# Kernel optimization log

Measured on AMD Instinct MI355X. Metric: run time of the kernel, lower is better.

## Reference

```python
import jax, jax.numpy as jnp
import numpy as np

N, E, D, ED, H = 50000, 640000, 128, 64, 128
EPS = 1e-5


def _bn(x, gamma, beta):
    # BatchNorm1d in training mode: batch stats over rows, biased variance
    mean = jnp.mean(x, axis=0)
    var = jnp.mean(jnp.square(x - mean), axis=0)
    return (x - mean) * jax.lax.rsqrt(var + EPS) * gamma + beta


def setup_inputs() -> dict:
    key = jax.random.key(0)
    ks = jax.random.split(key, 12)

    def lin(k, fan_in, fan_out):
        return jax.random.normal(k, (fan_in, fan_out), jnp.float32) / np.sqrt(fan_in)

    return {
        "h": jax.random.normal(ks[0], (N, D), jnp.float32),
        "edge_attr": jax.random.normal(ks[1], (E, ED), jnp.float32),
        # msg MLP: Linear(2D+ED->H), BN(H), ReLU, Linear(H->H)
        "W1": lin(ks[2], 2 * D + ED, H), "b1": jnp.zeros((H,), jnp.float32),
        "g1": jnp.ones((H,), jnp.float32), "be1": jnp.zeros((H,), jnp.float32),
        "W2": lin(ks[3], H, H), "b2": jnp.zeros((H,), jnp.float32),
        # upd MLP: Linear(D+H->H), BN(H), ReLU, Linear(H->D)
        "W3": lin(ks[4], D + H, H), "b3": jnp.zeros((H,), jnp.float32),
        "g2": jnp.ones((H,), jnp.float32), "be2": jnp.zeros((H,), jnp.float32),
        "W4": lin(ks[5], H, D), "b4": jnp.zeros((D,), jnp.float32),
        # residual LayerNorm
        "ln_g": jnp.ones((D,), jnp.float32), "ln_b": jnp.zeros((D,), jnp.float32),
        "edge_index": jax.random.randint(ks[6], (2, E), 0, N, jnp.int32),
        "num_nodes": N,
    }


def reference(h, edge_attr, W1, b1, g1, be1, W2, b2, W3, b3, g2, be2, W4, b4,
              ln_g, ln_b, edge_index, num_nodes):
    src, dst = edge_index[0], edge_index[1]
    # messages: MLP_msg(h_src || h_dst || e)  -> [E, H]
    msg_in = jnp.concatenate([h[src], h[dst], edge_attr], axis=-1)  # [E, 2D+ED]
    x = _bn(msg_in @ W1 + b1, g1, be1)
    messages = jax.nn.relu(x) @ W2 + b2
    # scatter-sum aggregate into dst nodes -> [N, H]
    agg = jax.ops.segment_sum(messages, dst, num_segments=num_nodes)
    # update: MLP_upd(h || agg) -> [N, D]
    u = jnp.concatenate([h, agg], axis=-1)
    y = _bn(u @ W3 + b3, g2, be2)
    h_new = jax.nn.relu(y) @ W4 + b4
    # residual + LayerNorm
    z = h + h_new
    mu = jnp.mean(z, axis=-1, keepdims=True)
    var = jnp.mean(jnp.square(z - mu), axis=-1, keepdims=True)
    return (z - mu) * jax.lax.rsqrt(var + EPS) * ln_g + ln_b
```

## Files before the change

kernel.cpp:

```cpp
#include <hip/hip_runtime.h>
#include <hip/hip_bf16.h>

#define EPS 1e-5f
#define DIMH 128
#define K1 320
#define K3 256

typedef __attribute__((ext_vector_type(8))) short bf16x8;
typedef __attribute__((ext_vector_type(4))) short bf16x4;
typedef __attribute__((ext_vector_type(4))) float f32x4;

#define MFMA(a, b, c) __builtin_amdgcn_mfma_f32_16x16x32_bf16(a, b, c, 0, 0, 0)

static __device__ __forceinline__ unsigned short f2bf(float f) {
    union { float f; unsigned u; } v; v.f = f;
    unsigned r = v.u + 0x7FFF + ((v.u >> 16) & 1);
    return (unsigned short)(r >> 16);
}

static __device__ __forceinline__ void gload16(const void* g, void* l) {
    __builtin_amdgcn_global_load_lds(
        (const __attribute__((address_space(1))) unsigned int*)g,
        (__attribute__((address_space(3))) unsigned int*)l, 16, 0, 0);
}

__global__ void k_prep_w(const float* __restrict__ W1, const float* __restrict__ W3,
                         const float* __restrict__ W4,
                         unsigned short* __restrict__ W1t, unsigned short* __restrict__ W3c,
                         unsigned short* __restrict__ W4t) {
    int t = blockIdx.x * 256 + threadIdx.x;
    if (t < K1 * 128) { int k = t / 128, n = t % 128; W1t[n * K1 + k] = f2bf(W1[t]); }
    if (t < 128 * 128) {
        int k = t / 128, n = t % 128;
        W4t[n * 128 + k] = f2bf(W4[t]);
        W3c[n * K3 + k] = f2bf(W3[t]);
    }
}

__global__ void k_hb(const float* __restrict__ h, unsigned short* __restrict__ hb, int total8) {
    int t = blockIdx.x * 256 + threadIdx.x;
    if (t < total8) {
        float4 a = *(const float4*)(h + (size_t)t * 8);
        float4 b = *(const float4*)(h + (size_t)t * 8 + 4);
        union { bf16x8 v; unsigned short s[8]; } u;
        u.s[0] = f2bf(a.x); u.s[1] = f2bf(a.y); u.s[2] = f2bf(a.z); u.s[3] = f2bf(a.w);
        u.s[4] = f2bf(b.x); u.s[5] = f2bf(b.y); u.s[6] = f2bf(b.z); u.s[7] = f2bf(b.w);
        *(bf16x8*)(hb + (size_t)t * 8) = u.v;
    }
}

__global__ void k_w23(const float* __restrict__ W2, const float* __restrict__ W3,
                      unsigned short* __restrict__ W3c) {
    int t = blockIdx.x * 256 + threadIdx.x;
    int j = t & 127, i = t >> 7;
    float s = 0.f;
    for (int k = 0; k < 128; ++k) s += W2[i * 128 + k] * W3[(128 + k) * 128 + j];
    W3c[j * K3 + 128 + i] = f2bf(s);
}

__global__ void k_cvec(const float* __restrict__ b2, const float* __restrict__ W3,
                       float* __restrict__ cvec) {
    int j = threadIdx.x;
    float s = 0.f;
    for (int k = 0; k < 128; ++k) s += b2[k] * W3[(128 + k) * 128 + j];
    cvec[j] = s;
}

__global__ void k_bn(const float* __restrict__ stats, const float* __restrict__ g,
                     const float* __restrict__ be, float* __restrict__ st, float cnt) {
    int c = threadIdx.x;
    float mean = stats[c] / cnt;
    float var = stats[128 + c] / cnt - mean * mean;
    float s = g[c] * rsqrtf(var + EPS);
    st[c] = s;
    st[128 + c] = be[c] - mean * s;
}

__global__ void k_deg(const int* __restrict__ dst, int* __restrict__ deg, int E) {
    int e = blockIdx.x * 256 + threadIdx.x;
    if (e < E) atomicAdd(&deg[dst[e]], 1);
}

__global__ void k_scan(const int* __restrict__ deg, int* __restrict__ offs,
                       int* __restrict__ cursor, int NN) {
    __shared__ int ps[1024];
    int t = threadIdx.x;
    int chunk = (NN + 1023) >> 10;
    int c0 = t * chunk;
    int s = 0;
    for (int i = 0; i < chunk; ++i) { int id = c0 + i; if (id < NN) s += deg[id]; }
    ps[t] = s; __syncthreads();
    for (int off = 1; off < 1024; off <<= 1) {
        int v = (t >= off) ? ps[t - off] : 0;
        __syncthreads();
        ps[t] += v;
        __syncthreads();
    }
    int run = t ? ps[t - 1] : 0;
    for (int i = 0; i < chunk; ++i) {
        int id = c0 + i;
        if (id < NN) { cursor[id] = run; run += deg[id]; offs[id] = run; }
    }
}

__global__ void k_scatter(const int* __restrict__ dst, int* __restrict__ cursor,
                          int* __restrict__ elist, int E) {
    int e = blockIdx.x * 256 + threadIdx.x;
    if (e < E) {
        int pos = atomicAdd(&cursor[dst[e]], 1);
        elist[pos] = e;
    }
}

__global__ __launch_bounds__(256, 3) void k_msg1(
    const unsigned short* __restrict__ hb, const float* __restrict__ ea,
    const int* __restrict__ src, const int* __restrict__ dst,
    const unsigned short* __restrict__ W1t, const float* __restrict__ b1,
    unsigned short* __restrict__ xout, float* __restrict__ stats) {
    __shared__ unsigned short As[64 * 128];
    __shared__ unsigned short Ad[64 * 128];
    __shared__ unsigned short Ae[64 * 64];
    int tid = threadIdx.x, lane = tid & 63, w = tid >> 6;
    int l15 = lane & 15, kq = lane >> 4;
    long e0 = (long)blockIdx.x * 64;

    bf16x8 bfr[10][2];
    {
        int n = (w << 5) + l15, kb = kq << 3;
#pragma unroll
        for (int nt = 0; nt < 2; ++nt) {
            const unsigned short* p = W1t + (size_t)(n + nt * 16) * K1 + kb;
#pragma unroll
            for (int ks = 0; ks < 10; ++ks) bfr[ks][nt] = *(const bf16x8*)(p + ks * 32);
        }
    }
    {
#pragma unroll
        for (int j = 0; j < 4; ++j) {
            int r4 = (w << 4) + j * 4;
            int row = r4 + kq;
            int u = l15 ^ (row & 7);
            long e = e0 + row;
            int sI = src[e], dI = dst[e];
            gload16(hb + (size_t)sI * 128 + u * 8, &As[r4 * 128]);
            gload16(hb + (size_t)dI * 128 + u * 8, &Ad[r4 * 128]);
        }
    }
    {
        int s8 = lane & 7, rq8 = lane >> 3;
#pragma unroll
        for (int p = 0; p < 2; ++p) {
            int row = (w << 4) + p * 8 + rq8;
            int u = (s8 ^ (row & 7)) << 3;
            const float* ep = ea + (size_t)(e0 + row) * 64 + u;
            float4 va = *(const float4*)ep;
            float4 vb = *(const float4*)(ep + 4);
            union { bf16x8 v; unsigned short s[8]; } uu;
            uu.s[0] = f2bf(va.x); uu.s[1] = f2bf(va.y); uu.s[2] = f2bf(va.z); uu.s[3] = f2bf(va.w);
            uu.s[4] = f2bf(vb.x); uu.s[5] = f2bf(vb.y); uu.s[6] = f2bf(vb.z); uu.s[7] = f2bf(vb.w);
            *(bf16x8*)&Ae[row * 64 + s8 * 8] = uu.v;
        }
    }
    __syncthreads();

    f32x4 acc[4][2] = {};
#pragma unroll
    for (int rg = 0; rg < 4; ++rg) {
        int a = rg * 16 + l15;
        int swz = a & 7;
        const unsigned short* pAs = As + a * 128;
        const unsigned short* pAd = Ad + a * 128;
        const unsigned short* pAe = Ae + a * 64;
#pragma unroll
        for (int ks = 0; ks < 4; ++ks) {
            bf16x8 af = *(const bf16x8*)(pAs + (((ks << 2) + kq) ^ swz) * 8);
            acc[rg][0] = MFMA(af, bfr[ks][0], acc[rg][0]);
            acc[rg][1] = MFMA(af, bfr[ks][1], acc[rg][1]);
        }
#pragma unroll
        for (int ks = 0; ks < 4; ++ks) {
            bf16x8 af = *(const bf16x8*)(pAd + (((ks << 2) + kq) ^ swz) * 8);
            acc[rg][0] = MFMA(af, bfr[4 + ks][0], acc[rg][0]);
            acc[rg][1] = MFMA(af, bfr[4 + ks][1], acc[rg][1]);
        }
#pragma unroll
        for (int ks = 0; ks < 2; ++ks) {
            bf16x8 af = *(const bf16x8*)(pAe + (((ks << 2) + kq) ^ swz) * 8);
            acc[rg][0] = MFMA(af, bfr[8 + ks][0], acc[rg][0]);
            acc[rg][1] = MFMA(af, bfr[8 + ks][1], acc[rg][1]);
        }
    }
    __syncthreads();
    unsigned short* xt = As;
    int c0 = (w << 5) + l15;
    float bias0 = b1[c0], bias1 = b1[c0 + 16];
    float ss0 = 0.f, ss1 = 0.f, sq0 = 0.f, sq1 = 0.f;
#pragma unroll
    for (int rg = 0; rg < 4; ++rg)
#pragma unroll
        for (int r = 0; r < 4; ++r) {
            int row = rg * 16 + (kq << 2) + r;
            float v0 = acc[rg][0][r] + bias0;
            float v1 = acc[rg][1][r] + bias1;
            ss0 += v0; sq0 += v0 * v0;
            ss1 += v1; sq1 += v1 * v1;
            xt[row * 128 + c0] = f2bf(v0);
            xt[row * 128 + c0 + 16] = f2bf(v1);
        }
    __syncthreads();
#pragma unroll
    for (int p = 0; p < 4; ++p) {
        int off8 = p * 2048 + tid * 8;
        *(bf16x8*)(xout + (size_t)e0 * 128 + off8) = *(const bf16x8*)(xt + off8);
    }
    ss0 += __shfl_xor(ss0, 16); ss0 += __shfl_xor(ss0, 32);
    sq0 += __shfl_xor(sq0, 16); sq0 += __shfl_xor(sq0, 32);
    ss1 += __shfl_xor(ss1, 16); ss1 += __shfl_xor(ss1, 32);
    sq1 += __shfl_xor(sq1, 16); sq1 += __shfl_xor(sq1, 32);
    if (lane < 16) {
        atomicAdd(&stats[c0], ss0);        atomicAdd(&stats[c0 + 16], ss1);
        atomicAdd(&stats[128 + c0], sq0);  atomicAdd(&stats[128 + c0 + 16], sq1);
    }
}

__global__ __launch_bounds__(256, 8) void k_agg(
    const unsigned short* __restrict__ x, const float* __restrict__ st,
    const int* __restrict__ offs, const int* __restrict__ deg,
    const int* __restrict__ elist, float* __restrict__ R, int NN) {
    int lane = threadIdx.x & 63, w = threadIdx.x >> 6;
    int n = blockIdx.x * 4 + w;
    if (n >= NN) return;
    int c = lane * 2;
    float s0 = st[c], s1 = st[c + 1], t0 = st[128 + c], t1 = st[128 + c + 1];
    int end = offs[n], i = end - deg[n];
    float a0 = 0.f, a1 = 0.f;
    for (; i + 3 < end; i += 4) {
        int e0 = elist[i], e1 = elist[i + 1], e2 = elist[i + 2], e3 = elist[i + 3];
        unsigned v0 = *(const unsigned*)(x + (size_t)e0 * DIMH + c);
        unsigned v1 = *(const unsigned*)(x + (size_t)e1 * DIMH + c);
        unsigned v2 = *(const unsigned*)(x + (size_t)e2 * DIMH + c);
        unsigned v3 = *(const unsigned*)(x + (size_t)e3 * DIMH + c);
        a0 += fmaxf(__uint_as_float(v0 << 16) * s0 + t0, 0.f);
        a1 += fmaxf(__uint_as_float(v0 & 0xffff0000u) * s1 + t1, 0.f);
        a0 += fmaxf(__uint_as_float(v1 << 16) * s0 + t0, 0.f);
        a1 += fmaxf(__uint_as_float(v1 & 0xffff0000u) * s1 + t1, 0.f);
        a0 += fmaxf(__uint_as_float(v2 << 16) * s0 + t0, 0.f);
        a1 += fmaxf(__uint_as_float(v2 & 0xffff0000u) * s1 + t1, 0.f);
        a0 += fmaxf(__uint_as_float(v3 << 16) * s0 + t0, 0.f);
        a1 += fmaxf(__uint_as_float(v3 & 0xffff0000u) * s1 + t1, 0.f);
    }
    for (; i < end; ++i) {
        int e0 = elist[i];
        unsigned v0 = *(const unsigned*)(x + (size_t)e0 * DIMH + c);
        a0 += fmaxf(__uint_as_float(v0 << 16) * s0 + t0, 0.f);
        a1 += fmaxf(__uint_as_float(v0 & 0xffff0000u) * s1 + t1, 0.f);
    }
    *(float2*)(R + (size_t)n * DIMH + c) = make_float2(a0, a1);
}

__global__ __launch_bounds__(256, 3) void k_upd1(
    const unsigned short* __restrict__ hb, const float* __restrict__ R,
    const unsigned short* __restrict__ W3c, const float* __restrict__ b3,
    const int* __restrict__ deg, const float* __restrict__ cvec,
    unsigned short* __restrict__ ypre, float* __restrict__ stats, int NN) {
    __shared__ unsigned short A[64 * K3];
    int tid = threadIdx.x, lane = tid & 63, w = tid >> 6;
    int n0 = blockIdx.x * 64;

    bf16x8 bfr[8][2];
    {
        int n = (w << 5) + (lane & 15), kb = (lane >> 4) << 3;
#pragma unroll
        for (int nt = 0; nt < 2; ++nt) {
            const unsigned short* p = W3c + (size_t)(n + nt * 16) * K3 + kb;
#pragma unroll
            for (int ks = 0; ks < 8; ++ks) bfr[ks][nt] = *(const bf16x8*)(p + ks * 32);
        }
    }
    {
        int c16 = tid & 15, r2 = tid >> 4;
#pragma unroll
        for (int rr = 0; rr < 4; ++rr) {
            int row = rr * 16 + r2;
            int node = n0 + row;
            bf16x8 vh = {};
            union { bf16x8 v8; unsigned short s8[8]; } ur;
            if (node < NN) {
                vh = *(const bf16x8*)(hb + (size_t)node * DIMH + c16 * 8);
                float4 r0 = *(const float4*)(R + (size_t)node * DIMH + c16 * 8);
                float4 r1 = *(const float4*)(R + (size_t)node * DIMH + c16 * 8 + 4);
                ur.s8[0] = f2bf(r0.x); ur.s8[1] = f2bf(r0.y); ur.s8[2] = f2bf(r0.z); ur.s8[3] = f2bf(r0.w);
                ur.s8[4] = f2bf(r1.x); ur.s8[5] = f2bf(r1.y); ur.s8[6] = f2bf(r1.z); ur.s8[7] = f2bf(r1.w);
            } else {
#pragma unroll
                for (int j = 0; j < 8; ++j) ur.s8[j] = 0;
            }
            int base = row * K3, sw = (row & 7) << 3;
            *(bf16x8*)&A[(base + c16 * 8) ^ sw] = vh;
            *(bf16x8*)&A[(base + 128 + c16 * 8) ^ sw] = ur.v8;
        }
    }
    __syncthreads();

    f32x4 acc[4][2] = {};
#pragma unroll
    for (int rg = 0; rg < 4; ++rg) {
        int arow = rg * 16 + (lane & 15);
        int base = arow * K3, sw = (arow & 7) << 3, kb = (lane >> 4) << 3;
#pragma unroll
        for (int ks = 0; ks < 8; ++ks) {
            bf16x8 af = *(const bf16x8*)&A[(base + ks * 32 + kb) ^ sw];
            acc[rg][0] = MFMA(af, bfr[ks][0], acc[rg][0]);
            acc[rg][1] = MFMA(af, bfr[ks][1], acc[rg][1]);
        }
    }
    int c0 = (w << 5) + (lane & 15);
    float bias0 = b3[c0], bias1 = b3[c0 + 16];
    float cv0 = cvec[c0], cv1 = cvec[c0 + 16];
    float ss[2] = {0.f, 0.f}, sq[2] = {0.f, 0.f};
#pragma unroll
    for (int rg = 0; rg < 4; ++rg)
#pragma unroll
        for (int r = 0; r < 4; ++r) {
            int node = n0 + rg * 16 + ((lane >> 4) << 2) + r;
            if (node < NN) {
                float dg = (float)deg[node];
                float v0 = acc[rg][0][r] + bias0 + dg * cv0;
                float v1 = acc[rg][1][r] + bias1 + dg * cv1;
                ss[0] += v0; sq[0] += v0 * v0;
                ss[1] += v1; sq[1] += v1 * v1;
                ypre[(size_t)node * DIMH + c0] = f2bf(v0);
                ypre[(size_t)node * DIMH + c0 + 16] = f2bf(v1);
            }
        }
#pragma unroll
    for (int nt = 0; nt < 2; ++nt) {
        ss[nt] += __shfl_xor(ss[nt], 16); ss[nt] += __shfl_xor(ss[nt], 32);
        sq[nt] += __shfl_xor(sq[nt], 16); sq[nt] += __shfl_xor(sq[nt], 32);
    }
    if (lane < 16) {
        atomicAdd(&stats[c0], ss[0]);        atomicAdd(&stats[c0 + 16], ss[1]);
        atomicAdd(&stats[128 + c0], sq[0]);  atomicAdd(&stats[128 + c0 + 16], sq[1]);
    }
}

__global__ __launch_bounds__(256, 2) void k_upd2(
    const unsigned short* __restrict__ ypre, const unsigned short* __restrict__ W4t,
    const float* __restrict__ b4, const float* __restrict__ st,
    const float* __restrict__ h, const float* __restrict__ lng,
    const float* __restrict__ lnb, float* __restrict__ out, int NN) {
    const int LDA = 136;
    __shared__ unsigned short A[64 * 136];
    __shared__ float sS[128], sT[128];
    __shared__ float rsum[64], rsq[64];
    int tid = threadIdx.x, lane = tid & 63, w = tid >> 6;
    int n0 = blockIdx.x * 64;
    if (tid < 128) { sS[tid] = st[tid]; sT[tid] = st[128 + tid]; }
    if (tid < 64) { rsum[tid] = 0.f; rsq[tid] = 0.f; }

    bf16x8 bfr[4][2];
    {
        int n = (w << 5) + (lane & 15), kb = (lane >> 4) << 3;
#pragma unroll
        for (int nt = 0; nt < 2; ++nt) {
            const unsigned short* p = W4t + (size_t)(n + nt * 16) * 128 + kb;
#pragma unroll
            for (int ks = 0; ks < 4; ++ks) bfr[ks][nt] = *(const bf16x8*)(p + ks * 32);
        }
    }
    __syncthreads();
    {
        int c16 = tid & 15, r2 = tid >> 4;
#pragma unroll
        for (int rr = 0; rr < 4; ++rr) {
            int row = rr * 16 + r2;
            int node = n0 + row;
            union { bf16x8 v8; unsigned short s[8]; } u;
            if (node < NN) {
                bf16x8 v = *(const bf16x8*)(ypre + (size_t)node * DIMH + c16 * 8);
#pragma unroll
                for (int j = 0; j < 8; ++j) {
                    int c = c16 * 8 + j;
                    union { unsigned uu; float f; } cvt; cvt.uu = ((unsigned)(unsigned short)v[j]) << 16;
                    float f = cvt.f * sS[c] + sT[c];
                    u.s[j] = f2bf(fmaxf(f, 0.f));
                }
            } else {
#pragma unroll
                for (int j = 0; j < 8; ++j) u.s[j] = 0;
            }
            *(bf16x8*)&A[row * LDA + c16 * 8] = u.v8;
        }
    }
    __syncthreads();

    f32x4 acc[4][2] = {};
#pragma unroll
    for (int rg = 0; rg < 4; ++rg) {
        int ab = (rg * 16 + (lane & 15)) * LDA + ((lane >> 4) << 3);
#pragma unroll
        for (int ks = 0; ks < 4; ++ks) {
            bf16x8 af = *(const bf16x8*)&A[ab + ks * 32];
            acc[rg][0] = MFMA(af, bfr[ks][0], acc[rg][0]);
            acc[rg][1] = MFMA(af, bfr[ks][1], acc[rg][1]);
        }
    }
    int c0 = (w << 5) + (lane & 15);
    float bias0 = b4[c0], bias1 = b4[c0 + 16];
    float z[4][2][4];
#pragma unroll
    for (int rg = 0; rg < 4; ++rg)
#pragma unroll
        for (int r = 0; r < 4; ++r) {
            int node = n0 + rg * 16 + ((lane >> 4) << 2) + r;
            float h0 = 0.f, h1 = 0.f;
            if (node < NN) {
                h0 = h[(size_t)node * DIMH + c0];
                h1 = h[(size_t)node * DIMH + c0 + 16];
            }
            z[rg][0][r] = acc[rg][0][r] + bias0 + h0;
            z[rg][1][r] = acc[rg][1][r] + bias1 + h1;
        }
#pragma unroll
    for (int rg = 0; rg < 4; ++rg)
#pragma unroll
        for (int r = 0; r < 4; ++r) {
            float ps = z[rg][0][r] + z[rg][1][r];
            float pq = z[rg][0][r] * z[rg][0][r] + z[rg][1][r] * z[rg][1][r];
#pragma unroll
            for (int m = 1; m < 16; m <<= 1) { ps += __shfl_xor(ps, m); pq += __shfl_xor(pq, m); }
            if ((lane & 15) == 0) {
                int row = rg * 16 + ((lane >> 4) << 2) + r;
                atomicAdd(&rsum[row], ps);
                atomicAdd(&rsq[row], pq);
            }
        }
    __syncthreads();
#pragma unroll
    for (int rg = 0; rg < 4; ++rg)
#pragma unroll
        for (int r = 0; r < 4; ++r) {
            int row = rg * 16 + ((lane >> 4) << 2) + r;
            int node = n0 + row;
            if (node < NN) {
                float mean = rsum[row] * (1.f / 128.f);
                float var = rsq[row] * (1.f / 128.f) - mean * mean;
                float rs = rsqrtf(var + EPS);
                float g0 = lng[c0], g1 = lng[c0 + 16];
                float be0 = lnb[c0], be1 = lnb[c0 + 16];
                out[(size_t)node * DIMH + c0] = (z[rg][0][r] - mean) * rs * g0 + be0;
                out[(size_t)node * DIMH + c0 + 16] = (z[rg][1][r] - mean) * rs * g1 + be1;
            }
        }
}

extern "C" void kernel_launch(void* const* d_in, const int* in_sizes, int n_in,
                              void* d_out, int out_size, void* d_ws, size_t ws_size,
                              hipStream_t stream) {
    const float* h   = (const float*)d_in[0];
    const float* ea  = (const float*)d_in[1];
    const float* W1  = (const float*)d_in[2];
    const float* b1  = (const float*)d_in[3];
    const float* g1  = (const float*)d_in[4];
    const float* be1 = (const float*)d_in[5];
    const float* W2  = (const float*)d_in[6];
    const float* b2  = (const float*)d_in[7];
    const float* W3  = (const float*)d_in[8];
    const float* b3  = (const float*)d_in[9];
    const float* g2  = (const float*)d_in[10];
    const float* be2 = (const float*)d_in[11];
    const float* W4  = (const float*)d_in[12];
    const float* b4  = (const float*)d_in[13];
    const float* lng = (const float*)d_in[14];
    const float* lnb = (const float*)d_in[15];
    const int* eidx  = (const int*)d_in[16];
    int NN = in_sizes[0] / DIMH;
    int E  = in_sizes[16] / 2;
    const int* src = eidx;
    const int* dst = eidx + E;

    char* ws = (char*)d_ws;
    size_t o = 0;
    unsigned short* W1t = (unsigned short*)(ws + o); o += 81920;
    unsigned short* W3c = (unsigned short*)(ws + o); o += 65536;
    unsigned short* W4t = (unsigned short*)(ws + o); o += 32768;
    float* cvec   = (float*)(ws + o); o += 512;
    float* stats1 = (float*)(ws + o); o += 1024;
    float* st1    = (float*)(ws + o); o += 1024;
    float* stats2 = (float*)(ws + o); o += 1024;
    float* st2    = (float*)(ws + o); o += 1024;
    int* deg    = (int*)(ws + o); o += 200192;
    int* offs   = (int*)(ws + o); o += 200192;
    int* cursor = (int*)(ws + o); o += 200192;
    int* elist  = (int*)(ws + o); o += (size_t)E * 4;
    unsigned short* hb = (unsigned short*)(ws + o); o += (size_t)NN * DIMH * 2;
    float* R = (float*)(ws + o); o += (size_t)NN * DIMH * 4;
    unsigned short* x = (unsigned short*)(ws + o);
    unsigned short* ypre = x;

    hipMemsetAsync(stats1, 0, 1024, stream);
    hipMemsetAsync(stats2, 0, 1024, stream);
    hipMemsetAsync(deg, 0, (size_t)NN * 4, stream);

    k_prep_w<<<(K1 * 128 + 255) / 256, 256, 0, stream>>>(W1, W3, W4, W1t, W3c, W4t);
    k_hb<<<(NN * DIMH / 8 + 255) / 256, 256, 0, stream>>>(h, hb, NN * DIMH / 8);
    k_w23<<<64, 256, 0, stream>>>(W2, W3, W3c);
    k_cvec<<<1, 128, 0, stream>>>(b2, W3, cvec);
    k_deg<<<(E + 255) / 256, 256, 0, stream>>>(dst, deg, E);
    k_scan<<<1, 1024, 0, stream>>>(deg, offs, cursor, NN);
    k_scatter<<<(E + 255) / 256, 256, 0, stream>>>(dst, cursor, elist, E);

    k_msg1<<<E / 64, 256, 0, stream>>>(hb, ea, src, dst, W1t, b1, x, stats1);
    k_bn<<<1, 128, 0, stream>>>(stats1, g1, be1, st1, (float)E);
    k_agg<<<(NN + 3) / 4, 256, 0, stream>>>(x, st1, offs, deg, elist, R, NN);

    int nb = (NN + 63) / 64;
    k_upd1<<<nb, 256, 0, stream>>>(hb, R, W3c, b3, deg, cvec, ypre, stats2, NN);
    k_bn<<<1, 128, 0, stream>>>(stats2, g2, be2, st2, (float)NN);
    k_upd2<<<nb, 256, 0, stream>>>(ypre, W4t, b4, st2, h, lng, lnb, (float*)d_out, NN);
}
```

Baseline: 812.6 us.

## Process edges in dst-sorted order so aggregation reads contiguous message rows

```diff
diff --git a/kernel.cpp b/kernel.cpp
--- a/kernel.cpp
+++ b/kernel.cpp
@@ -81,42 +81,69 @@
     if (e < E) atomicAdd(&deg[dst[e]], 1);
 }
 
-__global__ void k_scan(const int* __restrict__ deg, int* __restrict__ offs,
-                       int* __restrict__ cursor, int NN) {
-    __shared__ int ps[1024];
+__global__ void k_part(const int* __restrict__ deg, int* __restrict__ bsum, int NN) {
+    __shared__ int s[256];
+    int t = threadIdx.x, g = blockIdx.x * 256 + t;
+    s[t] = (g < NN) ? deg[g] : 0;
+    __syncthreads();
+    for (int o = 128; o > 0; o >>= 1) { if (t < o) s[t] += s[t + o]; __syncthreads(); }
+    if (t == 0) bsum[blockIdx.x] = s[0];
+}
+
+__global__ void k_scan2(const int* __restrict__ bsum, int* __restrict__ bpre, int nb) {
+    __shared__ int s[256];
     int t = threadIdx.x;
-    int chunk = (NN + 1023) >> 10;
-    int c0 = t * chunk;
-    int s = 0;
-    for (int i = 0; i < chunk; ++i) { int id = c0 + i; if (id < NN) s += deg[id]; }
-    ps[t] = s; __syncthreads();
-    for (int off = 1; off < 1024; off <<= 1) {
-        int v = (t >= off) ? ps[t - off] : 0;
+    int v = (t < nb) ? bsum[t] : 0;
+    s[t] = v; __syncthreads();
+    for (int o = 1; o < 256; o <<= 1) {
+        int u = (t >= o) ? s[t - o] : 0;
         __syncthreads();
-        ps[t] += v;
+        s[t] += u;
         __syncthreads();
     }
-    int run = t ? ps[t - 1] : 0;
-    for (int i = 0; i < chunk; ++i) {
-        int id = c0 + i;
-        if (id < NN) { cursor[id] = run; run += deg[id]; offs[id] = run; }
-    }
-}
-
-__global__ void k_scatter(const int* __restrict__ dst, int* __restrict__ cursor,
-                          int* __restrict__ elist, int E) {
+    if (t < nb) bpre[t] = s[t] - v;
+}
+
+__global__ void k_off(const int* __restrict__ deg, const int* __restrict__ bpre,
+                      int* __restrict__ offs, int* __restrict__ cursor, int NN) {
+    __shared__ int s[256];
+    int t = threadIdx.x, g = blockIdx.x * 256 + t;
+    int v = (g < NN) ? deg[g] : 0;
+    s[t] = v; __syncthreads();
+    for (int o = 1; o < 256; o <<= 1) {
+        int u = (t >= o) ? s[t - o] : 0;
+        __syncthreads();
+        s[t] += u;
+        __syncthreads();
+    }
+    if (g < NN) {
+        int incl = s[t] + bpre[blockIdx.x];
+        offs[g] = incl;
+        cursor[g] = incl - v;
+    }
+}
+
+__global__ void k_scatter(const int* __restrict__ src, const int* __restrict__ dst,
+                          int* __restrict__ cursor, int4* __restrict__ edge4, int E) {
     int e = blockIdx.x * 256 + threadIdx.x;
     if (e < E) {
-        int pos = atomicAdd(&cursor[dst[e]], 1);
-        elist[pos] = e;
-    }
-}
-
-__global__ __launch_bounds__(256, 3) void k_msg1(
-    const unsigned short* __restrict__ hb, const float* __restrict__ ea,
-    const int* __restrict__ src, const int* __restrict__ dst,
-    const unsigned short* __restrict__ W1t, const float* __restrict__ b1,
-    unsigned short* __restrict__ xout, float* __restrict__ stats) {
+        int d = dst[e];
+        int pos = atomicAdd(&cursor[d], 1);
+        edge4[pos] = make_int4(src[e], d, e, 0);
+    }
+}
+
+#define QSTEP(PTR, FIDX, BA, BB) do { \
+    bf16x8 af = *(const bf16x8*)((PTR) + ((((FIDX)) ^ swz) << 3)); \
+    acc[rg][0] = MFMA(af, BA, acc[rg][0]); \
+    acc[rg][1] = MFMA(af, BB, acc[rg][1]); } while (0)
+
+__global__ __launch_bounds__(256)
+__attribute__((amdgpu_waves_per_eu(2, 3)))
+void k_msg1(const unsigned short* __restrict__ hb, const float* __restrict__ ea,
+            const int4* __restrict__ edge4, const unsigned short* __restrict__ W1t,
+            const float* __restrict__ b1, unsigned short* __restrict__ xout,
+            float* __restrict__ stats) {
     __shared__ unsigned short As[64 * 128];
     __shared__ unsigned short Ad[64 * 128];
     __shared__ unsigned short Ae[64 * 64];
@@ -124,35 +151,45 @@
     int l15 = lane & 15, kq = lane >> 4;
     long e0 = (long)blockIdx.x * 64;
 
-    bf16x8 bfr[10][2];
+    bf16x8 B0a, B1a, B2a, B3a, B4a, B5a, B6a, B7a, B8a, B9a;
+    bf16x8 B0b, B1b, B2b, B3b, B4b, B5b, B6b, B7b, B8b, B9b;
     {
         int n = (w << 5) + l15, kb = kq << 3;
-#pragma unroll
-        for (int nt = 0; nt < 2; ++nt) {
-            const unsigned short* p = W1t + (size_t)(n + nt * 16) * K1 + kb;
-#pragma unroll
-            for (int ks = 0; ks < 10; ++ks) bfr[ks][nt] = *(const bf16x8*)(p + ks * 32);
-        }
-    }
-    {
-#pragma unroll
-        for (int j = 0; j < 4; ++j) {
-            int r4 = (w << 4) + j * 4;
-            int row = r4 + kq;
-            int u = l15 ^ (row & 7);
-            long e = e0 + row;
-            int sI = src[e], dI = dst[e];
-            gload16(hb + (size_t)sI * 128 + u * 8, &As[r4 * 128]);
-            gload16(hb + (size_t)dI * 128 + u * 8, &Ad[r4 * 128]);
-        }
+        const unsigned short* p0 = W1t + (size_t)n * K1 + kb;
+        const unsigned short* p1 = p0 + 16 * K1;
+        B0a = *(const bf16x8*)(p0 + 0);   B0b = *(const bf16x8*)(p1 + 0);
+        B1a = *(const bf16x8*)(p0 + 32);  B1b = *(const bf16x8*)(p1 + 32);
+        B2a = *(const bf16x8*)(p0 + 64);  B2b = *(const bf16x8*)(p1 + 64);
+        B3a = *(const bf16x8*)(p0 + 96);  B3b = *(const bf16x8*)(p1 + 96);
+        B4a = *(const bf16x8*)(p0 + 128); B4b = *(const bf16x8*)(p1 + 128);
+        B5a = *(const bf16x8*)(p0 + 160); B5b = *(const bf16x8*)(p1 + 160);
+        B6a = *(const bf16x8*)(p0 + 192); B6b = *(const bf16x8*)(p1 + 192);
+        B7a = *(const bf16x8*)(p0 + 224); B7b = *(const bf16x8*)(p1 + 224);
+        B8a = *(const bf16x8*)(p0 + 256); B8b = *(const bf16x8*)(p1 + 256);
+        B9a = *(const bf16x8*)(p0 + 288); B9b = *(const bf16x8*)(p1 + 288);
+    }
+    asm volatile("" : "+v"(B0a), "+v"(B1a), "+v"(B2a), "+v"(B3a), "+v"(B4a),
+                      "+v"(B5a), "+v"(B6a), "+v"(B7a), "+v"(B8a), "+v"(B9a));
+    asm volatile("" : "+v"(B0b), "+v"(B1b), "+v"(B2b), "+v"(B3b), "+v"(B4b),
+                      "+v"(B5b), "+v"(B6b), "+v"(B7b), "+v"(B8b), "+v"(B9b));
+
+#pragma unroll
+    for (int j = 0; j < 4; ++j) {
+        int r4 = (w << 4) + j * 4;
+        int row = r4 + kq;
+        int4 ei = edge4[e0 + row];
+        int u = l15 ^ (row & 7);
+        gload16(hb + (size_t)ei.x * 128 + u * 8, &As[r4 * 128]);
+        gload16(hb + (size_t)ei.y * 128 + u * 8, &Ad[r4 * 128]);
     }
     {
         int s8 = lane & 7, rq8 = lane >> 3;
 #pragma unroll
         for (int p = 0; p < 2; ++p) {
             int row = (w << 4) + p * 8 + rq8;
+            int eid = edge4[e0 + row].z;
             int u = (s8 ^ (row & 7)) << 3;
-            const float* ep = ea + (size_t)(e0 + row) * 64 + u;
+            const float* ep = ea + (size_t)eid * 64 + u;
             float4 va = *(const float4*)ep;
             float4 vb = *(const float4*)(ep + 4);
             union { bf16x8 v; unsigned short s[8]; } uu;
@@ -171,24 +208,16 @@
         const unsigned short* pAs = As + a * 128;
         const unsigned short* pAd = Ad + a * 128;
         const unsigned short* pAe = Ae + a * 64;
-#pragma unroll
-        for (int ks = 0; ks < 4; ++ks) {
-            bf16x8 af = *(const bf16x8*)(pAs + (((ks << 2) + kq) ^ swz) * 8);
-            acc[rg][0] = MFMA(af, bfr[ks][0], acc[rg][0]);
-            acc[rg][1] = MFMA(af, bfr[ks][1], acc[rg][1]);
-        }
-#pragma unroll
-        for (int ks = 0; ks < 4; ++ks) {
-            bf16x8 af = *(const bf16x8*)(pAd + (((ks << 2) + kq) ^ swz) * 8);
-            acc[rg][0] = MFMA(af, bfr[4 + ks][0], acc[rg][0]);
-            acc[rg][1] = MFMA(af, bfr[4 + ks][1], acc[rg][1]);
-        }
-#pragma unroll
-        for (int ks = 0; ks < 2; ++ks) {
-            bf16x8 af = *(const bf16x8*)(pAe + (((ks << 2) + kq) ^ swz) * 8);
-            acc[rg][0] = MFMA(af, bfr[8 + ks][0], acc[rg][0]);
-            acc[rg][1] = MFMA(af, bfr[8 + ks][1], acc[rg][1]);
-        }
+        QSTEP(pAs, (0 << 2) + kq, B0a, B0b);
+        QSTEP(pAs, (1 << 2) + kq, B1a, B1b);
+        QSTEP(pAs, (2 << 2) + kq, B2a, B2b);
+        QSTEP(pAs, (3 << 2) + kq, B3a, B3b);
+        QSTEP(pAd, (0 << 2) + kq, B4a, B4b);
+        QSTEP(pAd, (1 << 2) + kq, B5a, B5b);
+        QSTEP(pAd, (2 << 2) + kq, B6a, B6b);
+        QSTEP(pAd, (3 << 2) + kq, B7a, B7b);
+        QSTEP(pAe, (0 << 2) + kq, B8a, B8b);
+        QSTEP(pAe, (1 << 2) + kq, B9a, B9b);
     }
     __syncthreads();
     unsigned short* xt = As;
@@ -226,7 +255,7 @@
 __global__ __launch_bounds__(256, 8) void k_agg(
     const unsigned short* __restrict__ x, const float* __restrict__ st,
     const int* __restrict__ offs, const int* __restrict__ deg,
-    const int* __restrict__ elist, float* __restrict__ R, int NN) {
+    float* __restrict__ R, int NN) {
     int lane = threadIdx.x & 63, w = threadIdx.x >> 6;
     int n = blockIdx.x * 4 + w;
     if (n >= NN) return;
@@ -234,24 +263,16 @@
     float s0 = st[c], s1 = st[c + 1], t0 = st[128 + c], t1 = st[128 + c + 1];
     int end = offs[n], i = end - deg[n];
     float a0 = 0.f, a1 = 0.f;
-    for (; i + 3 < end; i += 4) {
-        int e0 = elist[i], e1 = elist[i + 1], e2 = elist[i + 2], e3 = elist[i + 3];
-        unsigned v0 = *(const unsigned*)(x + (size_t)e0 * DIMH + c);
-        unsigned v1 = *(const unsigned*)(x + (size_t)e1 * DIMH + c);
-        unsigned v2 = *(const unsigned*)(x + (size_t)e2 * DIMH + c);
-        unsigned v3 = *(const unsigned*)(x + (size_t)e3 * DIMH + c);
+    for (; i + 1 < end; i += 2) {
+        unsigned v0 = *(const unsigned*)(x + (size_t)i * DIMH + c);
+        unsigned v1 = *(const unsigned*)(x + (size_t)(i + 1) * DIMH + c);
         a0 += fmaxf(__uint_as_float(v0 << 16) * s0 + t0, 0.f);
         a1 += fmaxf(__uint_as_float(v0 & 0xffff0000u) * s1 + t1, 0.f);
         a0 += fmaxf(__uint_as_float(v1 << 16) * s0 + t0, 0.f);
         a1 += fmaxf(__uint_as_float(v1 & 0xffff0000u) * s1 + t1, 0.f);
-        a0 += fmaxf(__uint_as_float(v2 << 16) * s0 + t0, 0.f);
-        a1 += fmaxf(__uint_as_float(v2 & 0xffff0000u) * s1 + t1, 0.f);
-        a0 += fmaxf(__uint_as_float(v3 << 16) * s0 + t0, 0.f);
-        a1 += fmaxf(__uint_as_float(v3 & 0xffff0000u) * s1 + t1, 0.f);
-    }
-    for (; i < end; ++i) {
-        int e0 = elist[i];
-        unsigned v0 = *(const unsigned*)(x + (size_t)e0 * DIMH + c);
+    }
+    if (i < end) {
+        unsigned v0 = *(const unsigned*)(x + (size_t)i * DIMH + c);
         a0 += fmaxf(__uint_as_float(v0 << 16) * s0 + t0, 0.f);
         a1 += fmaxf(__uint_as_float(v0 & 0xffff0000u) * s1 + t1, 0.f);
     }
@@ -489,10 +510,12 @@
     float* st1    = (float*)(ws + o); o += 1024;
     float* stats2 = (float*)(ws + o); o += 1024;
     float* st2    = (float*)(ws + o); o += 1024;
+    int* bsum   = (int*)(ws + o); o += 1024;
+    int* bpre   = (int*)(ws + o); o += 1024;
     int* deg    = (int*)(ws + o); o += 200192;
     int* offs   = (int*)(ws + o); o += 200192;
     int* cursor = (int*)(ws + o); o += 200192;
-    int* elist  = (int*)(ws + o); o += (size_t)E * 4;
+    int4* edge4 = (int4*)(ws + o); o += (size_t)E * 16;
     unsigned short* hb = (unsigned short*)(ws + o); o += (size_t)NN * DIMH * 2;
     float* R = (float*)(ws + o); o += (size_t)NN * DIMH * 4;
     unsigned short* x = (unsigned short*)(ws + o);
@@ -502,17 +525,20 @@
     hipMemsetAsync(stats2, 0, 1024, stream);
     hipMemsetAsync(deg, 0, (size_t)NN * 4, stream);
 
+    int nb256 = (NN + 255) / 256;
     k_prep_w<<<(K1 * 128 + 255) / 256, 256, 0, stream>>>(W1, W3, W4, W1t, W3c, W4t);
     k_hb<<<(NN * DIMH / 8 + 255) / 256, 256, 0, stream>>>(h, hb, NN * DIMH / 8);
     k_w23<<<64, 256, 0, stream>>>(W2, W3, W3c);
     k_cvec<<<1, 128, 0, stream>>>(b2, W3, cvec);
     k_deg<<<(E + 255) / 256, 256, 0, stream>>>(dst, deg, E);
-    k_scan<<<1, 1024, 0, stream>>>(deg, offs, cursor, NN);
-    k_scatter<<<(E + 255) / 256, 256, 0, stream>>>(dst, cursor, elist, E);
-
-    k_msg1<<<E / 64, 256, 0, stream>>>(hb, ea, src, dst, W1t, b1, x, stats1);
+    k_part<<<nb256, 256, 0, stream>>>(deg, bsum, NN);
+    k_scan2<<<1, 256, 0, stream>>>(bsum, bpre, nb256);
+    k_off<<<nb256, 256, 0, stream>>>(deg, bpre, offs, cursor, NN);
+    k_scatter<<<(E + 255) / 256, 256, 0, stream>>>(src, dst, cursor, edge4, E);
+
+    k_msg1<<<E / 64, 256, 0, stream>>>(hb, ea, edge4, W1t, b1, x, stats1);
     k_bn<<<1, 128, 0, stream>>>(stats1, g1, be1, st1, (float)E);
-    k_agg<<<(NN + 3) / 4, 256, 0, stream>>>(x, st1, offs, deg, elist, R, NN);
+    k_agg<<<(NN + 3) / 4, 256, 0, stream>>>(x, st1, offs, deg, R, NN);
 
     int nb = (NN + 63) / 64;
     k_upd1<<<nb, 256, 0, stream>>>(hb, R, W3c, b3, deg, cvec, ypre, stats2, NN);
```

Result: faster. 709.1 us (-12.7%).
